# Kernel optimization log

Hardware: AMD Instinct MI355X
Metric: run time of the kernel (lower is better)

## Reference

```python
import jax, jax.numpy as jnp
import numpy as np

B, IN_DIM, FEAT_DIM, MEM_SIZE, HID, OUT_DIM = 2048, 2048, 256, 100000, 2048, 1024


def setup_inputs() -> dict:
    key = jax.random.key(0)
    ks = jax.random.split(key, 14)
    w = lambda k, shape: (jax.random.normal(k, shape, jnp.float32) * 0.02)
    return {
        "x": jax.random.normal(ks[0], (B, IN_DIM), jnp.float32),
        # feature extractor: IN_DIM -> 512 -> 256 -> FEAT_DIM
        "W1": w(ks[1], (IN_DIM, 512)), "b1": jnp.zeros((512,), jnp.float32),
        "W2": w(ks[2], (512, 256)),    "b2": jnp.zeros((256,), jnp.float32),
        "W3": w(ks[3], (256, FEAT_DIM)), "b3": jnp.zeros((FEAT_DIM,), jnp.float32),
        # external memory table
        "memory": jax.random.normal(ks[4], (MEM_SIZE, FEAT_DIM), jnp.float32),
        # task column: 2*FEAT_DIM -> HID -> HID -> OUT_DIM
        "Wt1": w(ks[5], (2 * FEAT_DIM, HID)), "bt1": jnp.zeros((HID,), jnp.float32),
        "Wt2": w(ks[6], (HID, HID)),          "bt2": jnp.zeros((HID,), jnp.float32),
        "Wo": w(ks[7], (HID, OUT_DIM)),       "bo": jnp.zeros((OUT_DIM,), jnp.float32),
    }


def reference(x, W1, b1, W2, b2, W3, b3, memory, Wt1, bt1, Wt2, bt2, Wo, bo):
    # ---- feature extractor MLP ----
    f = jax.nn.relu(x @ W1 + b1)
    f = jax.nn.relu(f @ W2 + b2)
    f = f @ W3 + b3                      # [B, FEAT_DIM]

    # ---- ExternalMemory.query ----
    # torch code detaches both features and memory before scoring (CPU/numba)
    fd = jax.lax.stop_gradient(f)
    md = jax.lax.stop_gradient(memory)
    bsz = f.shape[0]
    # scores[i] = -sum_{b,d} (f_bd - m_id)^2
    #           = -(B*||m_i||^2 - 2 m_i . sum_b f_b + sum||f||^2)
    f_sum = jnp.sum(fd, axis=0)                         # [D]
    f_sq = jnp.sum(fd * fd)                             # scalar
    m_sq = jnp.sum(md * md, axis=1)                     # [M]
    scores = -(bsz * m_sq - 2.0 * (md @ f_sum) + f_sq)  # [M]

    k = min(MEM_SIZE, bsz)  # == B here (required for the concat below)
    _, idx = jax.lax.top_k(scores, k)                   # descending, like torch.topk
    mem_out = memory[idx]                               # [B, FEAT_DIM] (grad flows to memory)

    # ---- concat + task column ----
    h = jnp.concatenate([f, mem_out], axis=-1)          # [B, 2*FEAT_DIM]
    h = jax.nn.relu(h @ Wt1 + bt1)
    h = jax.nn.relu(h @ Wt2 + bt2)
    return h @ Wo + bo                                  # [B, OUT_DIM]
```

## Files before the change

kernel.cpp:

```cpp
#include <hip/hip_runtime.h>

typedef unsigned int u32;
typedef unsigned long long u64;
typedef unsigned short u16;

typedef __attribute__((ext_vector_type(8))) short bf16x8;
typedef __attribute__((ext_vector_type(4))) float f32x4;

#define FEAT 256
#define MEMN 100000

#define OPAQ(x) asm volatile("" : "+v"(x))

static __device__ __forceinline__ u16 f2bf(float x){
  u32 u = __float_as_uint(x);
  u32 r = u + 0x7fffu + ((u >> 16) & 1u);
  return (u16)(r >> 16);
}

template<int RELU>
__global__ __launch_bounds__(512) void gemm_seq_k(const float* __restrict__ A,
                                                  const float* __restrict__ Bm,
                                                  const float* __restrict__ bias,
                                                  float* __restrict__ C,
                                                  int M, int N, int K){
  __shared__ float At[2][32][68];
  __shared__ float Bs[2][32][68];
  const int t = threadIdx.x;
  const int tx = t & 31, ty = t >> 5;
  const int bm = blockIdx.y << 6, bn = blockIdx.x << 6;
  float acc[4][2], mast[4][2];
  #pragma unroll
  for (int i = 0; i < 4; i++)
    #pragma unroll
    for (int j = 0; j < 2; j++){ acc[i][j] = 0.f; mast[i][j] = 0.f; }

  float pa[4], pb[4];
  #pragma unroll
  for (int i = 0; i < 4; i++){
    int o = t + (i << 9);
    pa[i] = A [(u64)(bm + (o >> 5)) * K + (o & 31)];
    pb[i] = Bm[(u64)((o >> 6)) * N + bn + (o & 63)];
  }
  #pragma unroll
  for (int i = 0; i < 4; i++){
    int o = t + (i << 9);
    At[0][o & 31][o >> 5] = pa[i];
    Bs[0][o >> 6][o & 63] = pb[i];
  }
  __syncthreads();

  int cur = 0;
  for (int kt = 0; kt < K; kt += 32){
    const int nxt = kt + 32;
    if (nxt < K){
      #pragma unroll
      for (int i = 0; i < 4; i++){
        int o = t + (i << 9);
        pa[i] = A [(u64)(bm + (o >> 5)) * K + nxt + (o & 31)];
        pb[i] = Bm[(u64)(nxt + (o >> 6)) * N + bn + (o & 63)];
      }
    }
    #pragma unroll
    for (int k = 0; k < 32; k++){
      float4 av = *reinterpret_cast<const float4*>(&At[cur][k][ty << 2]);
      float2 bv = *reinterpret_cast<const float2*>(&Bs[cur][k][tx << 1]);
      acc[0][0] = fmaf(av.x, bv.x, acc[0][0]); acc[0][1] = fmaf(av.x, bv.y, acc[0][1]);
      acc[1][0] = fmaf(av.y, bv.x, acc[1][0]); acc[1][1] = fmaf(av.y, bv.y, acc[1][1]);
      acc[2][0] = fmaf(av.z, bv.x, acc[2][0]); acc[2][1] = fmaf(av.z, bv.y, acc[2][1]);
      acc[3][0] = fmaf(av.w, bv.x, acc[3][0]); acc[3][1] = fmaf(av.w, bv.y, acc[3][1]);
    }
    if ((nxt % 384) == 0 || nxt == K){
      #pragma unroll
      for (int i = 0; i < 4; i++)
        #pragma unroll
        for (int j = 0; j < 2; j++){ mast[i][j] = mast[i][j] + acc[i][j]; acc[i][j] = 0.f; }
    }
    if (nxt < K){
      #pragma unroll
      for (int i = 0; i < 4; i++){
        int o = t + (i << 9);
        At[cur ^ 1][o & 31][o >> 5] = pa[i];
        Bs[cur ^ 1][o >> 6][o & 63] = pb[i];
      }
      __syncthreads();
      cur ^= 1;
    }
  }
  #pragma unroll
  for (int i = 0; i < 4; i++){
    int row = bm + (ty << 2) + i;
    #pragma unroll
    for (int j = 0; j < 2; j++){
      int col = bn + (tx << 1) + j;
      float v = mast[i][j] + bias[col];
      if (RELU) v = v > 0.f ? v : 0.f;
      C[(u64)row * N + col] = v;
    }
  }
}

__global__ __launch_bounds__(256) void fsum_seq_k(const float* __restrict__ f,
                                                  float* __restrict__ fsum){
  int d = threadIdx.x;
  float s = 0.f;
  for (int r = 0; r < 2048; r++) s += f[(u64)r * FEAT + d];
  fsum[d] = s;
}

__device__ __forceinline__ float block128_sq_avx512(const float4* base, int off, int swz){
  float e0[16], e1[16], f0[16], s16[16];
  #pragma unroll
  for (int j = 0; j < 8; j++){
    #pragma unroll
    for (int q = 0; q < 4; q++){
      float4 v = base[off + (((j << 2) + q) ^ swz)];
      float p0 = v.x * v.x, p1 = v.y * v.y, p2 = v.z * v.z, p3 = v.w * v.w;
      OPAQ(p0); OPAQ(p1); OPAQ(p2); OPAQ(p3);
      int l = q << 2;
      if (j == 0 || j == 4){ e0[l] = p0; e0[l+1] = p1; e0[l+2] = p2; e0[l+3] = p3; }
      else if (j == 1 || j == 5){ e0[l] += p0; e0[l+1] += p1; e0[l+2] += p2; e0[l+3] += p3; }
      else if (j == 2 || j == 6){ e1[l] = p0; e1[l+1] = p1; e1[l+2] = p2; e1[l+3] = p3; }
      else { e1[l] += p0; e1[l+1] += p1; e1[l+2] += p2; e1[l+3] += p3; }
    }
    if (j == 3){
      #pragma unroll
      for (int l = 0; l < 16; l++) f0[l] = e0[l] + e1[l];
    }
    if (j == 7){
      #pragma unroll
      for (int l = 0; l < 16; l++) s16[l] = f0[l] + (e0[l] + e1[l]);
    }
  }
  float h8[8], h4[4], h2[2];
  #pragma unroll
  for (int l = 0; l < 8; l++) h8[l] = s16[l] + s16[l + 8];
  #pragma unroll
  for (int l = 0; l < 4; l++) h4[l] = h8[l] + h8[l + 4];
  h2[0] = h4[0] + h4[2]; h2[1] = h4[1] + h4[3];
  return h2[0] + h2[1];
}

__global__ __launch_bounds__(256) void leaf_k(const float* __restrict__ f,
                                              float* __restrict__ lf){
  int b = blockIdx.x * 256 + threadIdx.x;
  lf[b] = block128_sq_avx512((const float4*)(f + (u64)b * 128), 0, 0);
}

__global__ __launch_bounds__(1024) void tree_k(const float* __restrict__ lf,
                                               float* __restrict__ fsq){
  __shared__ float sa[4096];
  __shared__ float sb[2048];
  int t = threadIdx.x;
  for (int i = t; i < 4096; i += 1024) sa[i] = lf[i];
  __syncthreads();
  float* src = sa; float* dst = sb;
  for (int len = 2048; len >= 1; len >>= 1){
    for (int i = t; i < len; i += 1024) dst[i] = src[2 * i] + src[2 * i + 1];
    __syncthreads();
    float* tmp = src; src = dst; dst = tmp;
  }
  if (t == 0) *fsq = src[0];
}

__global__ __launch_bounds__(64) void score_row_k(const float* __restrict__ mem,
                                                  const float* __restrict__ fsum,
                                                  const float* __restrict__ fsq_p,
                                                  u32* __restrict__ keys,
                                                  u32* __restrict__ hist,
                                                  u32* __restrict__ hist2){
  __shared__ __align__(16) float fs[256];
  __shared__ u32 lh2[256];
  const int t = threadIdx.x;
  #pragma unroll
  for (int i = 0; i < 4; i++){ fs[t + (i << 6)] = fsum[t + (i << 6)]; lh2[t + (i << 6)] = 0; }
  __syncthreads();
  const int row = (blockIdx.x << 6) + t;
  if (row < MEMN){
    const float4* rowp = (const float4*)(mem + (u64)row * FEAT);
    const float4* s4 = (const float4*)fs;
    float dpr[8];
    #pragma unroll
    for (int j = 0; j < 8; j++) dpr[j] = 0.f;
    #pragma unroll
    for (int kb = 0; kb < 64; kb++){
      float4 mv = rowp[kb];
      float4 fv = s4[kb];
      int j0 = (kb & 1) ? 4 : 0;
      dpr[j0 + 0] = fmaf(mv.x, fv.x, dpr[j0 + 0]);
      dpr[j0 + 1] = fmaf(mv.y, fv.y, dpr[j0 + 1]);
      dpr[j0 + 2] = fmaf(mv.z, fv.z, dpr[j0 + 2]);
      dpr[j0 + 3] = fmaf(mv.w, fv.w, dpr[j0 + 3]);
    }
    float r0 = block128_sq_avx512(rowp, 0, 0);
    float r1 = block128_sq_avx512(rowp, 32, 0);
    float msq = r0 + r1;
    float b0 = dpr[0] + dpr[4], b1 = dpr[1] + dpr[5];
    float b2 = dpr[2] + dpr[6], b3 = dpr[3] + dpr[7];
    float dp = (b0 + b1) + (b2 + b3);
    float t1 = 2048.0f * msq;
    float t2 = 2.0f * dp;
    float d3 = t1 - t2;  OPAQ(d3);
    float d4 = d3 + fsq_p[0];
    float s = -d4;
    u32 bb = __float_as_uint(s);
    u32 key = (bb & 0x80000000u) ? ~bb : (bb | 0x80000000u);
    keys[row] = key;
    atomicAdd(&hist[key >> 14], 1u);
    atomicAdd(&lh2[key >> 24], 1u);
  }
  __syncthreads();
  #pragma unroll
  for (int i = 0; i < 4; i++){
    u32 v = lh2[t + (i << 6)];
    if (v) atomicAdd(&hist2[t + (i << 6)], v);
  }
}

__global__ __launch_bounds__(1024) void find_T_k(const u32* __restrict__ hist,
                                                 const u32* __restrict__ hist2,
                                                 u32* __restrict__ Tbin){
  __shared__ u32 h2[256];
  __shared__ int sh_c;
  __shared__ u32 sh_run;
  __shared__ u32 sa[1024], sb[1024];
  int t = threadIdx.x;
  if (t < 256) h2[t] = hist2[t];
  __syncthreads();
  if (t == 0){
    u32 run = 0; int cstar = 0;
    for (int c = 255; c >= 0; c--){
      u32 v = h2[c];
      if (run + v >= 2048u){ cstar = c; break; }
      run += v;
    }
    sh_c = cstar; sh_run = run;
  }
  __syncthreads();
  int cstar = sh_c; u32 run = sh_run;
  sa[t] = hist[cstar * 1024 + t];
  __syncthreads();
  u32* src = sa; u32* dst = sb;
  for (int off = 1; off < 1024; off <<= 1){
    u32 v = src[t];
    if (t + off < 1024) v += src[t + off];
    dst[t] = v;
    __syncthreads();
    u32* tmp = src; src = dst; dst = tmp;
  }
  u32 suf  = src[t];
  u32 sufn = (t < 1023) ? src[t + 1] : 0u;
  if (run + suf >= 2048u && !(run + sufn >= 2048u)) *Tbin = (u32)(cstar * 1024 + t);
}

__global__ __launch_bounds__(256) void compact_k(const u32* __restrict__ keys,
                                                 const u32* __restrict__ Tbin,
                                                 u64* __restrict__ pk,
                                                 u32* __restrict__ counter){
  int i = blockIdx.x * 256 + threadIdx.x;
  if (i >= MEMN) return;
  u32 k = keys[i];
  if ((k >> 14) >= *Tbin){
    u32 p = atomicAdd(counter, 1u);
    if (p < 4096u) pk[p] = ((u64)k << 32) | (u32)(0xFFFFFFFFu - (u32)i);
  }
}

__global__ __launch_bounds__(1024) void sort_k(const u64* __restrict__ pkin,
                                               u32* __restrict__ idxo){
  __shared__ u64 k[4096];
  for (int i = threadIdx.x; i < 4096; i += 1024) k[i] = pkin[i];
  __syncthreads();
  for (int size = 2; size <= 4096; size <<= 1){
    for (int stride = size >> 1; stride; stride >>= 1){
      #pragma unroll 2
      for (int pp = 0; pp < 2; pp++){
        int p = threadIdx.x + pp * 1024;
        int i = ((p / stride) * (stride << 1)) + (p % stride);
        int j = i + stride;
        u64 a = k[i], b = k[j];
        bool desc_ok = (a >= b);
        bool up = ((i & size) == 0);
        if (up ? !desc_ok : desc_ok){ k[i] = b; k[j] = a; }
      }
      __syncthreads();
    }
  }
  for (int i = threadIdx.x; i < 2048; i += 1024) idxo[i] = 0xFFFFFFFFu - (u32)k[i];
}

__global__ __launch_bounds__(256) void build_h_k(const float* __restrict__ f,
                                                 const float* __restrict__ mem,
                                                 const u32* __restrict__ idx,
                                                 u16* __restrict__ h){
  int r = blockIdx.x, t = threadIdx.x;
  h[(u64)r * 512 + t] = f2bf(f[(u64)r * FEAT + t]);
  h[(u64)r * 512 + 256 + t] = f2bf(mem[(u64)idx[r] * FEAT + t]);
}

__global__ void convT_k(const float* __restrict__ W, u16* __restrict__ WT, int K, int N){
  __shared__ float tile[32][33];
  int tx = threadIdx.x, ty = threadIdx.y;
  int bk = blockIdx.y << 5, bn = blockIdx.x << 5;
  #pragma unroll
  for (int i = 0; i < 4; i++){
    int r = ty + (i << 3);
    tile[r][tx] = W[(u64)(bk + r) * N + bn + tx];
  }
  __syncthreads();
  #pragma unroll
  for (int i = 0; i < 4; i++){
    int n = ty + (i << 3);
    WT[(u64)(bn + n) * K + bk + tx] = f2bf(tile[tx][n]);
  }
}

static __device__ __forceinline__ void gl_lds16(const u16* g, u16* l){
  __builtin_amdgcn_global_load_lds((const __attribute__((address_space(1))) void*)g,
                                   (__attribute__((address_space(3))) void*)l, 16, 0, 0);
}

template<int RELU, int OUTBF>
__global__ __launch_bounds__(256) void gemm_bf16_k(const u16* __restrict__ A,
                                                   const u16* __restrict__ BT,
                                                   const float* __restrict__ bias,
                                                   void* __restrict__ Cout,
                                                   int M, int N, int K){
  __shared__ u16 As[128 * 32];
  __shared__ u16 Bs[128 * 32];
  const int t = threadIdx.x;
  const int w = t >> 6, lane = t & 63;
  const int bm = blockIdx.y << 7, bn = blockIdx.x << 7;
  f32x4 acc[4][4];
  #pragma unroll
  for (int i = 0; i < 4; i++)
    #pragma unroll
    for (int j = 0; j < 4; j++) acc[i][j] = (f32x4){0.f, 0.f, 0.f, 0.f};
  const int row0 = (w >> 1) << 6, col0 = (w & 1) << 6;
  for (int kt = 0; kt < K; kt += 32){
    #pragma unroll
    for (int j = 0; j < 2; j++){
      int e = (((j << 2) + w) << 9) + (lane << 3);
      int r = e >> 5, c = e & 31;
      gl_lds16(A  + (u64)(bm + r) * K + kt + c, As + (((j << 2) + w) << 9));
      gl_lds16(BT + (u64)(bn + r) * K + kt + c, Bs + (((j << 2) + w) << 9));
    }
    __syncthreads();
    bf16x8 af[4], bfr[4];
    #pragma unroll
    for (int i = 0; i < 4; i++){
      af[i]  = *(const bf16x8*)(As + (row0 + (i << 4) + (lane & 15)) * 32 + ((lane >> 4) << 3));
      bfr[i] = *(const bf16x8*)(Bs + (col0 + (i << 4) + (lane & 15)) * 32 + ((lane >> 4) << 3));
    }
    #pragma unroll
    for (int i = 0; i < 4; i++)
      #pragma unroll
      for (int j = 0; j < 4; j++)
        acc[i][j] = __builtin_amdgcn_mfma_f32_16x16x32_bf16(af[i], bfr[j], acc[i][j], 0, 0, 0);
    __syncthreads();
  }
  #pragma unroll
  for (int i = 0; i < 4; i++){
    #pragma unroll
    for (int j = 0; j < 4; j++){
      #pragma unroll
      for (int r = 0; r < 4; r++){
        int row = bm + row0 + (i << 4) + ((lane >> 4) << 2) + r;
        int col = bn + col0 + (j << 4) + (lane & 15);
        float v = acc[i][j][r] + bias[col];
        if (RELU) v = v > 0.f ? v : 0.f;
        if (OUTBF) ((u16*)Cout)[(u64)row * N + col] = f2bf(v);
        else       ((float*)Cout)[(u64)row * N + col] = v;
      }
    }
  }
}

extern "C" void kernel_launch(void* const* d_in, const int* in_sizes, int n_in,
                              void* d_out, int out_size, void* d_ws, size_t ws_size,
                              hipStream_t stream){
  const float* x   = (const float*)d_in[0];
  const float* W1  = (const float*)d_in[1];
  const float* b1  = (const float*)d_in[2];
  const float* W2  = (const float*)d_in[3];
  const float* b2  = (const float*)d_in[4];
  const float* W3  = (const float*)d_in[5];
  const float* b3  = (const float*)d_in[6];
  const float* mem = (const float*)d_in[7];
  const float* Wt1 = (const float*)d_in[8];
  const float* bt1 = (const float*)d_in[9];
  const float* Wt2 = (const float*)d_in[10];
  const float* bt2 = (const float*)d_in[11];
  const float* Wo  = (const float*)d_in[12];
  const float* bo  = (const float*)d_in[13];

  char* ws = (char*)d_ws;
  float* f1   = (float*)(ws + 0);
  u32*   keys = (u32*)  (ws + 0);
  u32*   hist = (u32*)  (ws + 0x080000);
  u32*   hist2= (u32*)  (ws + 0x180000);
  u32*   Tbin = (u32*)  (ws + 0x180000 + 1024);
  u32*   cnt  = (u32*)  (ws + 0x180000 + 1028);
  u64*   pk   = (u64*)  (ws + 0x180000 + 4096);
  u32*   idxo = (u32*)  (ws + 0x180000 + 40960);
  float* fsum = (float*)(ws + 0x180000 + 49152);
  float* lf   = (float*)(ws + 0x180000 + 50176);
  float* fsq  = (float*)(ws + 0x180000 + 66560);
  float* f2   = (float*)(ws + (4ull  << 20));
  float* f    = (float*)(ws + (6ull  << 20));
  u16*   h    = (u16*)  (ws + (8ull  << 20));
  u16*   W1T  = (u16*)  (ws + (10ull << 20));
  u16*   W2T  = (u16*)  (ws + (12ull << 20));
  u16*   WoT  = (u16*)  (ws + (20ull << 20));
  u16*   T1   = (u16*)  (ws + (24ull << 20));
  u16*   T2   = (u16*)  (ws + (32ull << 20));

  dim3 blk(256), blk512(512);
  gemm_seq_k<1><<<dim3(8, 32),  blk512, 0, stream>>>(x,  W1, b1, f1, 2048, 512, 2048);
  gemm_seq_k<1><<<dim3(4, 32),  blk512, 0, stream>>>(f1, W2, b2, f2, 2048, 256, 512);
  gemm_seq_k<0><<<dim3(4, 32),  blk512, 0, stream>>>(f2, W3, b3, f,  2048, 256, 256);
  hipMemsetAsync(hist, 0, 1048576, stream);
  hipMemsetAsync(ws + 0x180000, 0, 36864, stream);
  fsum_seq_k <<<dim3(1),    blk,        0, stream>>>(f, fsum);
  leaf_k     <<<dim3(16),   blk,        0, stream>>>(f, lf);
  tree_k     <<<dim3(1),    dim3(1024), 0, stream>>>(lf, fsq);
  score_row_k<<<dim3(1563), dim3(64),   0, stream>>>(mem, fsum, fsq, keys, hist, hist2);
  find_T_k   <<<dim3(1),    dim3(1024), 0, stream>>>(hist, hist2, Tbin);
  compact_k  <<<dim3(391),  blk,        0, stream>>>(keys, Tbin, pk, cnt);
  sort_k     <<<dim3(1),    dim3(1024), 0, stream>>>(pk, idxo);
  build_h_k<<<dim3(2048), blk, 0, stream>>>(f, mem, idxo, h);
  convT_k<<<dim3(64, 16), dim3(32, 8), 0, stream>>>(Wt1, W1T, 512,  2048);
  convT_k<<<dim3(64, 64), dim3(32, 8), 0, stream>>>(Wt2, W2T, 2048, 2048);
  convT_k<<<dim3(32, 64), dim3(32, 8), 0, stream>>>(Wo,  WoT, 2048, 1024);
  gemm_bf16_k<1, 1><<<dim3(16, 16), blk, 0, stream>>>(h,  W1T, bt1, T1, 2048, 2048, 512);
  gemm_bf16_k<1, 1><<<dim3(16, 16), blk, 0, stream>>>(T1, W2T, bt2, T2, 2048, 2048, 2048);
  gemm_bf16_k<0, 0><<<dim3(8, 16),  blk, 0, stream>>>(T2, WoT, bo, (float*)d_out, 2048, 1024, 2048);
}
```

Measured before the change: 492.9 us.

## Enlarge fp32 GEMM tiles, split score rows across lane pairs, spread fsum

The fp32 feature-extractor GEMM now computes a 128x64 tile per block, with a 4x4 register micro-tile per thread instead of 4x2. This improves reuse of shared-memory loads and halves the number of blocks. The memory-scoring kernel splits each 256-wide row between two adjacent lanes and combines the halves with xor shuffles, keeping the same summation tree so the scores stay bit-identical for top-k. fsum is spread over 4 blocks of 64 threads. The risks are lower occupancy and fewer blocks in the small GEMMs, plus strided per-lane access to memory rows in the score kernel.

```diff
diff --git a/kernel.cpp b/kernel.cpp
--- a/kernel.cpp
+++ b/kernel.cpp
@@ -24,30 +24,32 @@
                                                   const float* __restrict__ bias,
                                                   float* __restrict__ C,
                                                   int M, int N, int K){
-  __shared__ float At[2][32][68];
+  __shared__ float At[2][32][132];
   __shared__ float Bs[2][32][68];
   const int t = threadIdx.x;
-  const int tx = t & 31, ty = t >> 5;
-  const int bm = blockIdx.y << 6, bn = blockIdx.x << 6;
-  float acc[4][2], mast[4][2];
+  const int tx = t & 15, ty = t >> 4;
+  const int bm = blockIdx.y << 7, bn = blockIdx.x << 6;
+  float acc[4][4], mast[4][4];
   #pragma unroll
   for (int i = 0; i < 4; i++)
     #pragma unroll
-    for (int j = 0; j < 2; j++){ acc[i][j] = 0.f; mast[i][j] = 0.f; }
-
-  float pa[4], pb[4];
+    for (int j = 0; j < 4; j++){ acc[i][j] = 0.f; mast[i][j] = 0.f; }
+
+  float pa[8], pb[4];
+  #pragma unroll
+  for (int i = 0; i < 8; i++){
+    int o = t + (i << 9);
+    pa[i] = A[(u64)(bm + (o >> 5)) * K + (o & 31)];
+  }
   #pragma unroll
   for (int i = 0; i < 4; i++){
     int o = t + (i << 9);
-    pa[i] = A [(u64)(bm + (o >> 5)) * K + (o & 31)];
-    pb[i] = Bm[(u64)((o >> 6)) * N + bn + (o & 63)];
-  }
-  #pragma unroll
-  for (int i = 0; i < 4; i++){
-    int o = t + (i << 9);
-    At[0][o & 31][o >> 5] = pa[i];
-    Bs[0][o >> 6][o & 63] = pb[i];
-  }
+    pb[i] = Bm[(u64)(o >> 6) * N + bn + (o & 63)];
+  }
+  #pragma unroll
+  for (int i = 0; i < 8; i++){ int o = t + (i << 9); At[0][o & 31][o >> 5] = pa[i]; }
+  #pragma unroll
+  for (int i = 0; i < 4; i++){ int o = t + (i << 9); Bs[0][o >> 6][o & 63] = pb[i]; }
   __syncthreads();
 
   int cur = 0;
@@ -55,34 +57,40 @@
     const int nxt = kt + 32;
     if (nxt < K){
       #pragma unroll
+      for (int i = 0; i < 8; i++){
+        int o = t + (i << 9);
+        pa[i] = A[(u64)(bm + (o >> 5)) * K + nxt + (o & 31)];
+      }
+      #pragma unroll
       for (int i = 0; i < 4; i++){
         int o = t + (i << 9);
-        pa[i] = A [(u64)(bm + (o >> 5)) * K + nxt + (o & 31)];
         pb[i] = Bm[(u64)(nxt + (o >> 6)) * N + bn + (o & 63)];
       }
     }
     #pragma unroll
     for (int k = 0; k < 32; k++){
       float4 av = *reinterpret_cast<const float4*>(&At[cur][k][ty << 2]);
-      float2 bv = *reinterpret_cast<const float2*>(&Bs[cur][k][tx << 1]);
+      float4 bv = *reinterpret_cast<const float4*>(&Bs[cur][k][tx << 2]);
       acc[0][0] = fmaf(av.x, bv.x, acc[0][0]); acc[0][1] = fmaf(av.x, bv.y, acc[0][1]);
+      acc[0][2] = fmaf(av.x, bv.z, acc[0][2]); acc[0][3] = fmaf(av.x, bv.w, acc[0][3]);
       acc[1][0] = fmaf(av.y, bv.x, acc[1][0]); acc[1][1] = fmaf(av.y, bv.y, acc[1][1]);
+      acc[1][2] = fmaf(av.y, bv.z, acc[1][2]); acc[1][3] = fmaf(av.y, bv.w, acc[1][3]);
       acc[2][0] = fmaf(av.z, bv.x, acc[2][0]); acc[2][1] = fmaf(av.z, bv.y, acc[2][1]);
+      acc[2][2] = fmaf(av.z, bv.z, acc[2][2]); acc[2][3] = fmaf(av.z, bv.w, acc[2][3]);
       acc[3][0] = fmaf(av.w, bv.x, acc[3][0]); acc[3][1] = fmaf(av.w, bv.y, acc[3][1]);
+      acc[3][2] = fmaf(av.w, bv.z, acc[3][2]); acc[3][3] = fmaf(av.w, bv.w, acc[3][3]);
     }
     if ((nxt % 384) == 0 || nxt == K){
       #pragma unroll
       for (int i = 0; i < 4; i++)
         #pragma unroll
-        for (int j = 0; j < 2; j++){ mast[i][j] = mast[i][j] + acc[i][j]; acc[i][j] = 0.f; }
+        for (int j = 0; j < 4; j++){ mast[i][j] = mast[i][j] + acc[i][j]; acc[i][j] = 0.f; }
     }
     if (nxt < K){
       #pragma unroll
-      for (int i = 0; i < 4; i++){
-        int o = t + (i << 9);
-        At[cur ^ 1][o & 31][o >> 5] = pa[i];
-        Bs[cur ^ 1][o >> 6][o & 63] = pb[i];
-      }
+      for (int i = 0; i < 8; i++){ int o = t + (i << 9); At[cur ^ 1][o & 31][o >> 5] = pa[i]; }
+      #pragma unroll
+      for (int i = 0; i < 4; i++){ int o = t + (i << 9); Bs[cur ^ 1][o >> 6][o & 63] = pb[i]; }
       __syncthreads();
       cur ^= 1;
     }
@@ -91,8 +99,8 @@
   for (int i = 0; i < 4; i++){
     int row = bm + (ty << 2) + i;
     #pragma unroll
-    for (int j = 0; j < 2; j++){
-      int col = bn + (tx << 1) + j;
+    for (int j = 0; j < 4; j++){
+      int col = bn + (tx << 2) + j;
       float v = mast[i][j] + bias[col];
       if (RELU) v = v > 0.f ? v : 0.f;
       C[(u64)row * N + col] = v;
@@ -100,9 +108,9 @@
   }
 }
 
-__global__ __launch_bounds__(256) void fsum_seq_k(const float* __restrict__ f,
-                                                  float* __restrict__ fsum){
-  int d = threadIdx.x;
+__global__ __launch_bounds__(64) void fsum_seq_k(const float* __restrict__ f,
+                                                 float* __restrict__ fsum){
+  int d = (blockIdx.x << 6) + threadIdx.x;
   float s = 0.f;
   for (int r = 0; r < 2048; r++) s += f[(u64)r * FEAT + d];
   fsum[d] = s;
@@ -163,58 +171,93 @@
   if (t == 0) *fsq = src[0];
 }
 
-__global__ __launch_bounds__(64) void score_row_k(const float* __restrict__ mem,
-                                                  const float* __restrict__ fsum,
-                                                  const float* __restrict__ fsq_p,
-                                                  u32* __restrict__ keys,
-                                                  u32* __restrict__ hist,
-                                                  u32* __restrict__ hist2){
+__global__ __launch_bounds__(256) void score_row_k(const float* __restrict__ mem,
+                                                   const float* __restrict__ fsum,
+                                                   const float* __restrict__ fsq_p,
+                                                   u32* __restrict__ keys,
+                                                   u32* __restrict__ hist,
+                                                   u32* __restrict__ hist2){
   __shared__ __align__(16) float fs[256];
   __shared__ u32 lh2[256];
   const int t = threadIdx.x;
-  #pragma unroll
-  for (int i = 0; i < 4; i++){ fs[t + (i << 6)] = fsum[t + (i << 6)]; lh2[t + (i << 6)] = 0; }
-  __syncthreads();
-  const int row = (blockIdx.x << 6) + t;
-  if (row < MEMN){
+  fs[t] = fsum[t];
+  lh2[t] = 0;
+  __syncthreads();
+  const int sub = t & 1;
+  const int row = (blockIdx.x << 7) + (t >> 1);
+  float key_s = 0.f; bool live = (row < MEMN);
+  if (live){
     const float4* rowp = (const float4*)(mem + (u64)row * FEAT);
     const float4* s4 = (const float4*)fs;
-    float dpr[8];
-    #pragma unroll
-    for (int j = 0; j < 8; j++) dpr[j] = 0.f;
-    #pragma unroll
-    for (int kb = 0; kb < 64; kb++){
-      float4 mv = rowp[kb];
-      float4 fv = s4[kb];
-      int j0 = (kb & 1) ? 4 : 0;
-      dpr[j0 + 0] = fmaf(mv.x, fv.x, dpr[j0 + 0]);
-      dpr[j0 + 1] = fmaf(mv.y, fv.y, dpr[j0 + 1]);
-      dpr[j0 + 2] = fmaf(mv.z, fv.z, dpr[j0 + 2]);
-      dpr[j0 + 3] = fmaf(mv.w, fv.w, dpr[j0 + 3]);
-    }
-    float r0 = block128_sq_avx512(rowp, 0, 0);
-    float r1 = block128_sq_avx512(rowp, 32, 0);
-    float msq = r0 + r1;
-    float b0 = dpr[0] + dpr[4], b1 = dpr[1] + dpr[5];
-    float b2 = dpr[2] + dpr[6], b3 = dpr[3] + dpr[7];
+    float dpr[4];
+    #pragma unroll
+    for (int j = 0; j < 4; j++) dpr[j] = 0.f;
+    float msqh[2];
+    #pragma unroll
+    for (int blk = 0; blk < 2; blk++){
+      const int off = blk << 5;
+      float e0L[8], e1L[8], f0L[8], s16L[8];
+      #pragma unroll
+      for (int j = 0; j < 8; j++){
+        #pragma unroll
+        for (int cs = 0; cs < 2; cs++){
+          int kb = off + (j << 2) + sub + (cs << 1);
+          float4 v = rowp[kb];
+          float4 fv = s4[kb];
+          float p0 = v.x * v.x, p1 = v.y * v.y, p2 = v.z * v.z, p3 = v.w * v.w;
+          OPAQ(p0); OPAQ(p1); OPAQ(p2); OPAQ(p3);
+          int li = cs << 2;
+          if (j == 0 || j == 4){ e0L[li] = p0; e0L[li+1] = p1; e0L[li+2] = p2; e0L[li+3] = p3; }
+          else if (j == 1 || j == 5){ e0L[li] += p0; e0L[li+1] += p1; e0L[li+2] += p2; e0L[li+3] += p3; }
+          else if (j == 2 || j == 6){ e1L[li] = p0; e1L[li+1] = p1; e1L[li+2] = p2; e1L[li+3] = p3; }
+          else { e1L[li] += p0; e1L[li+1] += p1; e1L[li+2] += p2; e1L[li+3] += p3; }
+          dpr[0] = fmaf(v.x, fv.x, dpr[0]);
+          dpr[1] = fmaf(v.y, fv.y, dpr[1]);
+          dpr[2] = fmaf(v.z, fv.z, dpr[2]);
+          dpr[3] = fmaf(v.w, fv.w, dpr[3]);
+        }
+        if (j == 3){
+          #pragma unroll
+          for (int l = 0; l < 8; l++) f0L[l] = e0L[l] + e1L[l];
+        }
+        if (j == 7){
+          #pragma unroll
+          for (int l = 0; l < 8; l++) s16L[l] = f0L[l] + (e0L[l] + e1L[l]);
+        }
+      }
+      float h8L[4], oth[4], h4v[4];
+      #pragma unroll
+      for (int l = 0; l < 4; l++) h8L[l] = s16L[l] + s16L[4 + l];
+      #pragma unroll
+      for (int l = 0; l < 4; l++) oth[l] = __shfl_xor(h8L[l], 1);
+      #pragma unroll
+      for (int l = 0; l < 4; l++) h4v[l] = h8L[l] + oth[l];
+      float h2a = h4v[0] + h4v[2], h2b = h4v[1] + h4v[3];
+      msqh[blk] = h2a + h2b;
+    }
+    float msq = msqh[0] + msqh[1];
+    float od[4];
+    #pragma unroll
+    for (int i = 0; i < 4; i++) od[i] = __shfl_xor(dpr[i], 1);
+    float b0 = dpr[0] + od[0], b1 = dpr[1] + od[1];
+    float b2 = dpr[2] + od[2], b3 = dpr[3] + od[3];
     float dp = (b0 + b1) + (b2 + b3);
     float t1 = 2048.0f * msq;
     float t2 = 2.0f * dp;
     float d3 = t1 - t2;  OPAQ(d3);
     float d4 = d3 + fsq_p[0];
-    float s = -d4;
-    u32 bb = __float_as_uint(s);
+    key_s = -d4;
+  }
+  if (live && sub == 0){
+    u32 bb = __float_as_uint(key_s);
     u32 key = (bb & 0x80000000u) ? ~bb : (bb | 0x80000000u);
     keys[row] = key;
     atomicAdd(&hist[key >> 14], 1u);
     atomicAdd(&lh2[key >> 24], 1u);
   }
   __syncthreads();
-  #pragma unroll
-  for (int i = 0; i < 4; i++){
-    u32 v = lh2[t + (i << 6)];
-    if (v) atomicAdd(&hist2[t + (i << 6)], v);
-  }
+  u32 v = lh2[t];
+  if (v) atomicAdd(&hist2[t], v);
 }
 
 __global__ __launch_bounds__(1024) void find_T_k(const u32* __restrict__ hist,
@@ -416,18 +459,18 @@
   u16*   T2   = (u16*)  (ws + (32ull << 20));
 
   dim3 blk(256), blk512(512);
-  gemm_seq_k<1><<<dim3(8, 32),  blk512, 0, stream>>>(x,  W1, b1, f1, 2048, 512, 2048);
-  gemm_seq_k<1><<<dim3(4, 32),  blk512, 0, stream>>>(f1, W2, b2, f2, 2048, 256, 512);
-  gemm_seq_k<0><<<dim3(4, 32),  blk512, 0, stream>>>(f2, W3, b3, f,  2048, 256, 256);
+  gemm_seq_k<1><<<dim3(8, 16), blk512, 0, stream>>>(x,  W1, b1, f1, 2048, 512, 2048);
+  gemm_seq_k<1><<<dim3(4, 16), blk512, 0, stream>>>(f1, W2, b2, f2, 2048, 256, 512);
+  gemm_seq_k<0><<<dim3(4, 16), blk512, 0, stream>>>(f2, W3, b3, f,  2048, 256, 256);
   hipMemsetAsync(hist, 0, 1048576, stream);
   hipMemsetAsync(ws + 0x180000, 0, 36864, stream);
-  fsum_seq_k <<<dim3(1),    blk,        0, stream>>>(f, fsum);
-  leaf_k     <<<dim3(16),   blk,        0, stream>>>(f, lf);
-  tree_k     <<<dim3(1),    dim3(1024), 0, stream>>>(lf, fsq);
-  score_row_k<<<dim3(1563), dim3(64),   0, stream>>>(mem, fsum, fsq, keys, hist, hist2);
-  find_T_k   <<<dim3(1),    dim3(1024), 0, stream>>>(hist, hist2, Tbin);
-  compact_k  <<<dim3(391),  blk,        0, stream>>>(keys, Tbin, pk, cnt);
-  sort_k     <<<dim3(1),    dim3(1024), 0, stream>>>(pk, idxo);
+  fsum_seq_k <<<dim3(4),   dim3(64),   0, stream>>>(f, fsum);
+  leaf_k     <<<dim3(16),  blk,        0, stream>>>(f, lf);
+  tree_k     <<<dim3(1),   dim3(1024), 0, stream>>>(lf, fsq);
+  score_row_k<<<dim3(782), blk,        0, stream>>>(mem, fsum, fsq, keys, hist, hist2);
+  find_T_k   <<<dim3(1),   dim3(1024), 0, stream>>>(hist, hist2, Tbin);
+  compact_k  <<<dim3(391), blk,        0, stream>>>(keys, Tbin, pk, cnt);
+  sort_k     <<<dim3(1),   dim3(1024), 0, stream>>>(pk, idxo);
   build_h_k<<<dim3(2048), blk, 0, stream>>>(f, mem, idxo, h);
   convT_k<<<dim3(64, 16), dim3(32, 8), 0, stream>>>(Wt1, W1T, 512,  2048);
   convT_k<<<dim3(64, 64), dim3(32, 8), 0, stream>>>(Wt2, W2T, 2048, 2048);
```

Measured after the change: 534.7 us. +8.5%, slower.
